# Kernel tuning notes

Measured on AMD Instinct MI355X. Metric: run time of the kernel, lower is better.

## Reference

```python
import jax, jax.numpy as jnp
import numpy as np

N = 8192
IN_F = 512
OUT_F = 512
ALPHA = 0.2  # leaky relu slope


def setup_inputs() -> dict:
    key = jax.random.key(0)
    k1, k2, k3, k4, k5 = jax.random.split(key, 5)
    inp = jax.random.normal(k1, (N, IN_F), dtype=jnp.float32)
    adj = jax.random.randint(k2, (N, N), 0, 2, dtype=jnp.int32)
    # linear1: [in, out] + bias
    W1 = jax.random.normal(k3, (IN_F, OUT_F), dtype=jnp.float32) * (1.0 / np.sqrt(IN_F))
    b1 = jnp.zeros((OUT_F,), dtype=jnp.float32)
    # linear2: maps 2*out -> 1; split into the two halves acting on h_i and h_j
    a = jax.random.normal(k4, (2 * OUT_F,), dtype=jnp.float32) * (1.0 / np.sqrt(2 * OUT_F))
    a1 = a[:OUT_F]
    a2 = a[OUT_F:]
    b2 = jnp.zeros((), dtype=jnp.float32)
    return {"inp": inp, "adj": adj, "W1": W1, "b1": b1, "a1": a1, "a2": a2, "b2": b2}


def reference(inp, adj, W1, b1, a1, a2, b2):
    h = inp @ W1 + b1  # [N, out]
    # linear2(cat(h_i, h_j)) == h_i@a1 + h_j@a2 + b2 -> avoids the N*N*2F tensor
    e = jax.nn.leaky_relu((h @ a1)[:, None] + (h @ a2)[None, :] + b2, ALPHA)  # [N, N]
    attention = jnp.where(adj > 0, e, jnp.float32(-1e12))
    attention = jax.nn.softmax(attention, axis=1)
    h_prime = attention @ h  # [N, out]
    return jax.nn.elu(h_prime)  # concat=True
```

## Files before the change

### kernel.cpp

```cpp
#include <hip/hip_runtime.h>
#include <hip/hip_bf16.h>
#include <stdint.h>

#define NR 8192
#define FD 512
#define BM 64

typedef __attribute__((ext_vector_type(8))) short s8v;
typedef __attribute__((ext_vector_type(4))) float f32x4;

static __device__ __forceinline__ short bf16_rtne(float x) {
    union { float f; uint32_t u; } v; v.f = x;
    uint32_t r = (v.u + 0x7FFFu + ((v.u >> 16) & 1u)) >> 16;
    return (short)r;
}
static __device__ __forceinline__ float bf16_to_f32(short s) {
    union { uint32_t u; float f; } v; v.u = ((uint32_t)(uint16_t)s) << 16;
    return v.f;
}

__global__ void k_prepack(const int* __restrict__ adj,
                          unsigned long long* __restrict__ bm) {
    const int lane = threadIdx.x & 63;
    const int wv   = threadIdx.x >> 6;
    const int gid  = blockIdx.x * 4 + wv;
    const int row  = gid >> 2;
    const int seg  = (gid & 3) * 2048;
    const int* p   = adj + (size_t)row * NR + seg + lane;
    unsigned long long* o = bm + (((size_t)row * NR + seg) >> 6);
#pragma unroll
    for (int g = 0; g < 8; ++g) {
        unsigned long long b0 = __ballot(p[g * 256]       != 0);
        unsigned long long b1 = __ballot(p[g * 256 + 64]  != 0);
        unsigned long long b2 = __ballot(p[g * 256 + 128] != 0);
        unsigned long long b3 = __ballot(p[g * 256 + 192] != 0);
        unsigned long long vs = (lane == 0) ? b0 : (lane == 1) ? b1
                              : (lane == 2) ? b2 : b3;
        if (lane < 4) o[g * 4 + lane] = vs;
    }
}

__global__ void k_convert(const float* __restrict__ in, short* __restrict__ out) {
    int i = blockIdx.x * blockDim.x + threadIdx.x;
    float4 v = ((const float4*)in)[i];
    short4 s;
    s.x = bf16_rtne(v.x); s.y = bf16_rtne(v.y);
    s.z = bf16_rtne(v.z); s.w = bf16_rtne(v.w);
    ((short4*)out)[i] = s;
}

__global__ void k_w1t(const float* __restrict__ W1, short* __restrict__ W1T) {
    int i = blockIdx.x * 256 + threadIdx.x;
    int k = i & 511, n = i >> 9;
    W1T[(size_t)n * 512 + k] = bf16_rtne(W1[(size_t)k * 512 + n]);
}

__launch_bounds__(256)
__global__ void k_gemm_h(const short* __restrict__ A,
                         const short* __restrict__ BT,
                         const float* __restrict__ b1,
                         short* __restrict__ H,
                         short* __restrict__ HT3)
{
    const int lane = threadIdx.x & 63;
    const int wn   = threadIdx.x >> 6;
    const int m    = lane & 15;
    const int q    = lane >> 4;
    const int r0   = blockIdx.x * 32;
    const int c0   = blockIdx.y * 128 + wn * 32;

    f32x4 acc[2][2] = {};
#pragma unroll 1
    for (int k0 = 0; k0 < 512; k0 += 32) {
        s8v a[2], b[2];
#pragma unroll
        for (int rt = 0; rt < 2; ++rt)
            a[rt] = *(const s8v*)(A + (size_t)(r0 + rt * 16 + m) * 512 + k0 + q * 8);
#pragma unroll
        for (int nt = 0; nt < 2; ++nt)
            b[nt] = *(const s8v*)(BT + (size_t)(c0 + nt * 16 + m) * 512 + k0 + q * 8);
#pragma unroll
        for (int rt = 0; rt < 2; ++rt)
#pragma unroll
            for (int nt = 0; nt < 2; ++nt)
                acc[rt][nt] = __builtin_amdgcn_mfma_f32_16x16x32_bf16(a[rt], b[nt], acc[rt][nt], 0, 0, 0);
    }
    float b1v[2];
#pragma unroll
    for (int nt = 0; nt < 2; ++nt) b1v[nt] = b1[c0 + nt * 16 + m];

#pragma unroll
    for (int rt = 0; rt < 2; ++rt)
#pragma unroll
        for (int nt = 0; nt < 2; ++nt) {
            int col = c0 + nt * 16 + m;
            short4 hp;
#pragma unroll
            for (int r = 0; r < 4; ++r) {
                int row = r0 + rt * 16 + q * 4 + r;
                short hv = bf16_rtne(acc[rt][nt][r] + b1v[nt]);
                H[(size_t)row * 512 + col] = hv;
                ((short*)&hp)[r] = hv;
            }
            size_t off = (size_t)blockIdx.x * 16384
                       + (size_t)(blockIdx.y * 2 + (wn >> 1)) * 2048
                       + (size_t)((wn * 2 + nt) & 3) * 512
                       + (rt * 2 + (q >> 1)) * 128
                       + m * 8 + (q & 1) * 4;
            *(short4*)(HT3 + off) = hp;
        }
}

__global__ void k_f1f2(const short* __restrict__ H, const float* __restrict__ a1,
                       const float* __restrict__ a2, const float* __restrict__ b2,
                       float* __restrict__ f1, float* __restrict__ f2s)
{
    const int lane = threadIdx.x & 63;
    const int row  = blockIdx.x * 4 + (threadIdx.x >> 6);
    s8v hv = *(const s8v*)(H + (size_t)row * 512 + lane * 8);
    float4 a1l = ((const float4*)(a1 + lane * 8))[0];
    float4 a1h = ((const float4*)(a1 + lane * 8))[1];
    float4 a2l = ((const float4*)(a2 + lane * 8))[0];
    float4 a2h = ((const float4*)(a2 + lane * 8))[1];
    float hf[8];
#pragma unroll
    for (int i = 0; i < 8; ++i) hf[i] = bf16_to_f32(hv[i]);
    float s1 = hf[0] * a1l.x + hf[1] * a1l.y + hf[2] * a1l.z + hf[3] * a1l.w
             + hf[4] * a1h.x + hf[5] * a1h.y + hf[6] * a1h.z + hf[7] * a1h.w;
    float s2 = hf[0] * a2l.x + hf[1] * a2l.y + hf[2] * a2l.z + hf[3] * a2l.w
             + hf[4] * a2h.x + hf[5] * a2h.y + hf[6] * a2h.z + hf[7] * a2h.w;
#pragma unroll
    for (int o = 32; o > 0; o >>= 1) {
        s1 += __shfl_xor(s1, o);
        s2 += __shfl_xor(s2, o);
    }
    if (lane == 0) {
        f1[row]  = s1;
        f2s[row] = s2 + b2[0];
    }
}

__launch_bounds__(512, 2)
__global__ void k_attn(const uint32_t* __restrict__ bm,
                       const short* __restrict__ HT3,
                       const float* __restrict__ f1,
                       const float* __restrict__ f2s,
                       float* __restrict__ nump,
                       float* __restrict__ denomp)
{
    __shared__ __align__(16) short wt[2][BM * 256];
    __shared__ __align__(16) short bbuf[8][2][2048];

    const int t    = threadIdx.x;
    const int lane = t & 63;
    const int w    = t >> 6;
    const int m    = lane & 15;
    const int q    = lane >> 4;

    const int js   = blockIdx.x & 1;
    const int band = blockIdx.x >> 1;
    const int r0   = band * BM;
    const int jb0  = js * 4096;
    const int jt0  = js * 128;

    const int prow = t >> 3;
    const int jg   = t & 7;

    const float f1v = f1[r0 + prow];
    const uint32_t* bmrow = bm + (size_t)(r0 + prow) * 256 + js * 128;
    const float* f2base = f2s + jb0;

    f32x4 acc[4][4] = {};
    float dsum = 0.f;

#define GAT_DMA(KT)                                                            \
    {                                                                          \
        const short* src_ = HT3 + (size_t)(jt0 + (KT)) * 16384 + w * 2048;     \
        short* dst_ = &bbuf[w][(KT) & 1][0];                                   \
        _Pragma("unroll")                                                      \
        for (int b_ = 0; b_ < 4; ++b_) {                                       \
            __builtin_amdgcn_global_load_lds(                                  \
                (const __attribute__((address_space(1))) int*)                 \
                    (src_ + b_ * 512 + lane * 8),                              \
                (__attribute__((address_space(3))) int*)(dst_ + b_ * 512),     \
                16, 0, 0);                                                     \
        }                                                                      \
    }

#define GAT_WGEN(CH, P)                                                        \
    {                                                                          \
        uint4 mwa_ = *(const uint4*)(bmrow + (CH) * 8);                        \
        uint4 mwb_ = *(const uint4*)(bmrow + (CH) * 8 + 4);                    \
        uint32_t m8_[8] = {mwa_.x, mwa_.y, mwa_.z, mwa_.w,                     \
                           mwb_.x, mwb_.y, mwb_.z, mwb_.w};                    \
        _Pragma("unroll")                                                      \
        for (int k_ = 0; k_ < 4; ++k_) {                                       \
            const int u_ = jg + 8 * k_;                                        \
            uint32_t byte_ = (m8_[(jg >> 2) + 2 * k_] >> ((jg & 3) * 8)) & 0xFFu; \
            float4 fa_ = *(const float4*)(f2base + (CH) * 256 + u_ * 8);       \
            float4 fb_ = *(const float4*)(f2base + (CH) * 256 + u_ * 8 + 4);   \
            s8v wv_;                                                           \
            const float* ff_ = (const float*)&fa_;                             \
            _Pragma("unroll")                                                  \
            for (int jj = 0; jj < 4; ++jj) {                                   \
                float s_ = f1v + ff_[jj];                                      \
                float e_ = __expf(fmaxf(s_, 0.2f * s_));                       \
                float x_ = ((byte_ >> jj) & 1u) ? e_ : 0.f;                    \
                dsum += x_; wv_[jj] = bf16_rtne(x_);                           \
            }                                                                  \
            const float* fg_ = (const float*)&fb_;                            \
            _Pragma("unroll")                                                  \
            for (int jj = 0; jj < 4; ++jj) {                                   \
                float s_ = f1v + fg_[jj];                                      \
                float e_ = __expf(fmaxf(s_, 0.2f * s_));                       \
                float x_ = ((byte_ >> (4 + jj)) & 1u) ? e_ : 0.f;              \
                dsum += x_; wv_[4 + jj] = bf16_rtne(x_);                       \
            }                                                                  \
            *(s8v*)&wt[P][prow * 256 + ((u_ ^ (prow & 7)) << 3)] = wv_;        \
        }                                                                      \
    }

    GAT_DMA(0)
    GAT_WGEN(0, 0)
    __syncthreads();

    int kt = 0;
#pragma unroll 1
    for (int ch = 0; ch < 16; ++ch) {
        const int p = ch & 1;
#pragma unroll
        for (int kk = 0; kk < 8; ++kk, ++kt) {
            const int bufc = kt & 1;
            GAT_DMA((kt + 1) & 127)
            __builtin_amdgcn_s_waitcnt(0x0F74);
            s8v af[4];
#pragma unroll
            for (int i = 0; i < 4; ++i)
                af[i] = *(const s8v*)&wt[p][(i * 16 + m) * 256
                                            + (((kk * 4 + q) ^ (m & 7)) << 3)];
            const short* bb = &bbuf[w][bufc][0];
#pragma unroll
            for (int nt = 0; nt < 4; ++nt) {
                s8v b = *(const s8v*)&bb[nt * 512 + q * 128 + m * 8];
#pragma unroll
                for (int i = 0; i < 4; ++i)
                    acc[i][nt] = __builtin_amdgcn_mfma_f32_16x16x32_bf16(af[i], b, acc[i][nt], 0, 0, 0);
            }
        }
        if (ch < 15) GAT_WGEN(ch + 1, p ^ 1)
        __syncthreads();
    }
#undef GAT_DMA
#undef GAT_WGEN

    dsum += __shfl_xor(dsum, 1);
    dsum += __shfl_xor(dsum, 2);
    dsum += __shfl_xor(dsum, 4);
    if (jg == 0) denomp[(size_t)js * NR + r0 + prow] = dsum;

    float* np = nump + (size_t)js * NR * FD;
#pragma unroll
    for (int i = 0; i < 4; ++i)
#pragma unroll
        for (int nt = 0; nt < 4; ++nt)
#pragma unroll
            for (int r = 0; r < 4; ++r) {
                int row = r0 + i * 16 + q * 4 + r;
                int col = w * 64 + nt * 16 + m;
                np[(size_t)row * FD + col] = acc[i][nt][r];
            }
}

__global__ void k_combine(const float* __restrict__ nump,
                          const float* __restrict__ denomp,
                          float* __restrict__ out)
{
    size_t e = ((size_t)blockIdx.x * 256 + threadIdx.x) * 4;
    int row = (int)(e >> 9);
    float4 n0 = *(const float4*)(nump + e);
    float4 n1 = *(const float4*)(nump + (size_t)NR * FD + e);
    float d = denomp[row] + denomp[NR + row];
    float inv = 1.0f / d;
    float4 o;
    o.x = (n0.x + n1.x) * inv;
    o.y = (n0.y + n1.y) * inv;
    o.z = (n0.z + n1.z) * inv;
    o.w = (n0.w + n1.w) * inv;
    o.x = (o.x > 0.f) ? o.x : (__expf(o.x) - 1.f);
    o.y = (o.y > 0.f) ? o.y : (__expf(o.y) - 1.f);
    o.z = (o.z > 0.f) ? o.z : (__expf(o.z) - 1.f);
    o.w = (o.w > 0.f) ? o.w : (__expf(o.w) - 1.f);
    *(float4*)(out + e) = o;
}

extern "C" void kernel_launch(void* const* d_in, const int* in_sizes, int n_in,
                              void* d_out, int out_size, void* d_ws, size_t ws_size,
                              hipStream_t stream) {
    const float* inp = (const float*)d_in[0];
    const int*   adj = (const int*)d_in[1];
    const float* W1  = (const float*)d_in[2];
    const float* b1  = (const float*)d_in[3];
    const float* a1  = (const float*)d_in[4];
    const float* a2  = (const float*)d_in[5];
    const float* b2  = (const float*)d_in[6];
    float* out = (float*)d_out;

    short*    inp_bf = (short*)d_ws;
    short*    w1t    = inp_bf + (size_t)NR * FD;
    short*    h      = w1t + (size_t)FD * FD;
    short*    ht3    = h + (size_t)NR * FD;
    uint32_t* bmw    = (uint32_t*)(ht3 + (size_t)FD * NR);
    float*    f1     = (float*)(bmw + (size_t)NR * 256);
    float*    f2s    = f1 + NR;
    float*    nump   = f2s + NR;
    float*    denomp = nump + (size_t)2 * NR * FD;

    k_prepack<<<NR, 256, 0, stream>>>(adj, (unsigned long long*)bmw);
    k_convert<<<(NR * FD / 4) / 256, 256, 0, stream>>>(inp, inp_bf);
    k_w1t<<<(FD * FD) / 256, 256, 0, stream>>>(W1, w1t);
    dim3 g1(NR / 32, FD / 128);
    k_gemm_h<<<g1, 256, 0, stream>>>(inp_bf, w1t, b1, h, ht3);
    k_f1f2<<<NR / 4, 256, 0, stream>>>(h, a1, a2, b2, f1, f2s);
    k_attn<<<128 * 2, 512, 0, stream>>>(bmw, ht3, f1, f2s, nump, denomp);
    k_combine<<<(NR * FD / 4) / 256, 256, 0, stream>>>(nump, denomp, out);
}
```

Baseline: 513.6 us.

## Load B fragments directly into registers and interleave weight generation with MFMAs

The B operand (transposed h tiles) no longer goes through an LDS staging buffer via global_load_lds with explicit waitcnt. Each lane now loads its fragments straight into registers, prefetching two k-steps ahead. The next chunk's attention-weight generation (exp, mask, bf16 pack into LDS) is split into four units and spread across the MFMA k-loop instead of running after it. This aims to hide the exp and global-load latency behind matrix work and to cut LDS traffic, at the cost of higher register pressure under launch_bounds(512,2).

```diff
diff --git a/kernel.cpp b/kernel.cpp
--- a/kernel.cpp
+++ b/kernel.cpp
@@ -149,7 +149,6 @@
                        float* __restrict__ denomp)
 {
     __shared__ __align__(16) short wt[2][BM * 256];
-    __shared__ __align__(16) short bbuf[8][2][2048];
 
     const int t    = threadIdx.x;
     const int lane = t & 63;
@@ -173,85 +172,102 @@
     f32x4 acc[4][4] = {};
     float dsum = 0.f;
 
-#define GAT_DMA(KT)                                                            \
+#define GAT_BLOAD(DST, KT)                                                     \
     {                                                                          \
-        const short* src_ = HT3 + (size_t)(jt0 + (KT)) * 16384 + w * 2048;     \
-        short* dst_ = &bbuf[w][(KT) & 1][0];                                   \
+        const short* s_ = HT3 + (size_t)(jt0 + (KT)) * 16384 + w * 2048        \
+                        + q * 128 + m * 8;                                     \
+        DST[0] = *(const s8v*)(s_);                                            \
+        DST[1] = *(const s8v*)(s_ + 512);                                      \
+        DST[2] = *(const s8v*)(s_ + 1024);                                     \
+        DST[3] = *(const s8v*)(s_ + 1536);                                     \
+    }
+
+#define GAT_WUNIT(U, BYTE, FA, FB, P)                                          \
+    {                                                                          \
+        s8v wv_;                                                               \
+        const float* ff_ = (const float*)&(FA);                                \
         _Pragma("unroll")                                                      \
-        for (int b_ = 0; b_ < 4; ++b_) {                                       \
-            __builtin_amdgcn_global_load_lds(                                  \
-                (const __attribute__((address_space(1))) int*)                 \
-                    (src_ + b_ * 512 + lane * 8),                              \
-                (__attribute__((address_space(3))) int*)(dst_ + b_ * 512),     \
-                16, 0, 0);                                                     \
+        for (int jj = 0; jj < 4; ++jj) {                                       \
+            float s_ = f1v + ff_[jj];                                          \
+            float e_ = __expf(fmaxf(s_, 0.2f * s_));                           \
+            float x_ = (((BYTE) >> jj) & 1u) ? e_ : 0.f;                       \
+            dsum += x_; wv_[jj] = bf16_rtne(x_);                               \
         }                                                                      \
-    }
-
-#define GAT_WGEN(CH, P)                                                        \
-    {                                                                          \
-        uint4 mwa_ = *(const uint4*)(bmrow + (CH) * 8);                        \
-        uint4 mwb_ = *(const uint4*)(bmrow + (CH) * 8 + 4);                    \
-        uint32_t m8_[8] = {mwa_.x, mwa_.y, mwa_.z, mwa_.w,                     \
-                           mwb_.x, mwb_.y, mwb_.z, mwb_.w};                    \
+        const float* fg_ = (const float*)&(FB);                               \
         _Pragma("unroll")                                                      \
-        for (int k_ = 0; k_ < 4; ++k_) {                                       \
-            const int u_ = jg + 8 * k_;                                        \
-            uint32_t byte_ = (m8_[(jg >> 2) + 2 * k_] >> ((jg & 3) * 8)) & 0xFFu; \
-            float4 fa_ = *(const float4*)(f2base + (CH) * 256 + u_ * 8);       \
-            float4 fb_ = *(const float4*)(f2base + (CH) * 256 + u_ * 8 + 4);   \
-            s8v wv_;                                                           \
-            const float* ff_ = (const float*)&fa_;                             \
-            _Pragma("unroll")                                                  \
-            for (int jj = 0; jj < 4; ++jj) {                                   \
-                float s_ = f1v + ff_[jj];                                      \
-                float e_ = __expf(fmaxf(s_, 0.2f * s_));                       \
-                float x_ = ((byte_ >> jj) & 1u) ? e_ : 0.f;                    \
-                dsum += x_; wv_[jj] = bf16_rtne(x_);                           \
-            }                                                                  \
-            const float* fg_ = (const float*)&fb_;                            \
-            _Pragma("unroll")                                                  \
-            for (int jj = 0; jj < 4; ++jj) {                                   \
-                float s_ = f1v + fg_[jj];                                      \
-                float e_ = __expf(fmaxf(s_, 0.2f * s_));                       \
-                float x_ = ((byte_ >> (4 + jj)) & 1u) ? e_ : 0.f;              \
-                dsum += x_; wv_[4 + jj] = bf16_rtne(x_);                       \
-            }                                                                  \
-            *(s8v*)&wt[P][prow * 256 + ((u_ ^ (prow & 7)) << 3)] = wv_;        \
+        for (int jj = 0; jj < 4; ++jj) {                                       \
+            float s_ = f1v + fg_[jj];                                          \
+            float e_ = __expf(fmaxf(s_, 0.2f * s_));                           \
+            float x_ = (((BYTE) >> (4 + jj)) & 1u) ? e_ : 0.f;                 \
+            dsum += x_; wv_[4 + jj] = bf16_rtne(x_);                           \
         }                                                                      \
-    }
-
-    GAT_DMA(0)
-    GAT_WGEN(0, 0)
+        *(s8v*)&wt[P][prow * 256 + (((U) ^ (prow & 7)) << 3)] = wv_;           \
+    }
+
+    {
+        uint4 mwa_ = *(const uint4*)(bmrow);
+        uint4 mwb_ = *(const uint4*)(bmrow + 4);
+        uint32_t m8_[8] = {mwa_.x, mwa_.y, mwa_.z, mwa_.w,
+                           mwb_.x, mwb_.y, mwb_.z, mwb_.w};
+#pragma unroll
+        for (int k_ = 0; k_ < 4; ++k_) {
+            const int u_ = jg + 8 * k_;
+            uint32_t byte_ = (m8_[(jg >> 2) + 2 * k_] >> ((jg & 3) * 8)) & 0xFFu;
+            float4 fa_ = *(const float4*)(f2base + u_ * 8);
+            float4 fb_ = *(const float4*)(f2base + u_ * 8 + 4);
+            GAT_WUNIT(u_, byte_, fa_, fb_, 0)
+        }
+    }
+    s8v breg[2][4];
+    GAT_BLOAD(breg[0], 0)
+    GAT_BLOAD(breg[1], 1)
     __syncthreads();
 
     int kt = 0;
 #pragma unroll 1
     for (int ch = 0; ch < 16; ++ch) {
         const int p = ch & 1;
+        const int chn = (ch + 1) & 15;
+        uint4 mwa_ = *(const uint4*)(bmrow + chn * 8);
+        uint4 mwb_ = *(const uint4*)(bmrow + chn * 8 + 4);
+        float4 fa_[4], fb_[4];
+#pragma unroll
+        for (int k_ = 0; k_ < 4; ++k_) {
+            const int u_ = jg + 8 * k_;
+            fa_[k_] = *(const float4*)(f2base + chn * 256 + u_ * 8);
+            fb_[k_] = *(const float4*)(f2base + chn * 256 + u_ * 8 + 4);
+        }
+        uint32_t m8_[8] = {mwa_.x, mwa_.y, mwa_.z, mwa_.w,
+                           mwb_.x, mwb_.y, mwb_.z, mwb_.w};
+
 #pragma unroll
         for (int kk = 0; kk < 8; ++kk, ++kt) {
-            const int bufc = kt & 1;
-            GAT_DMA((kt + 1) & 127)
-            __builtin_amdgcn_s_waitcnt(0x0F74);
+            const int e = kk & 1;
+            s8v bn[4];
+            GAT_BLOAD(bn, (kt + 2) & 127)
             s8v af[4];
 #pragma unroll
             for (int i = 0; i < 4; ++i)
                 af[i] = *(const s8v*)&wt[p][(i * 16 + m) * 256
                                             + (((kk * 4 + q) ^ (m & 7)) << 3)];
-            const short* bb = &bbuf[w][bufc][0];
-#pragma unroll
-            for (int nt = 0; nt < 4; ++nt) {
-                s8v b = *(const s8v*)&bb[nt * 512 + q * 128 + m * 8];
+#pragma unroll
+            for (int nt = 0; nt < 4; ++nt)
 #pragma unroll
                 for (int i = 0; i < 4; ++i)
-                    acc[i][nt] = __builtin_amdgcn_mfma_f32_16x16x32_bf16(af[i], b, acc[i][nt], 0, 0, 0);
+                    acc[i][nt] = __builtin_amdgcn_mfma_f32_16x16x32_bf16(af[i], breg[e][nt], acc[i][nt], 0, 0, 0);
+            if (kk >= 2 && kk <= 5 && ch < 15) {
+                const int k_ = kk - 2;
+                const int u_ = jg + 8 * k_;
+                uint32_t byte_ = (m8_[(jg >> 2) + 2 * k_] >> ((jg & 3) * 8)) & 0xFFu;
+                GAT_WUNIT(u_, byte_, fa_[k_], fb_[k_], p ^ 1)
             }
+#pragma unroll
+            for (int nt = 0; nt < 4; ++nt) breg[e][nt] = bn[nt];
         }
-        if (ch < 15) GAT_WGEN(ch + 1, p ^ 1)
         __syncthreads();
     }
-#undef GAT_DMA
-#undef GAT_WGEN
+#undef GAT_BLOAD
+#undef GAT_WUNIT
 
     dsum += __shfl_xor(dsum, 1);
     dsum += __shfl_xor(dsum, 2);
```

Result: no change. 505.0 us (-1.7%).
